# Performance work log

Hardware: AMD Instinct MI355X
Metric: run time of the kernel (lower is better)

Reference implementation:

```python
import jax, jax.numpy as jnp
import numpy as np
import math

HEADS = 16
SPH = 64      # size_per_head
KEY = 64      # key_size (defaults to size_per_head)
EMB = 1024
STEP = 3


def extract_seq_patches(x, kernel_size, step):
    # x: [B, L, D] -> [B, L, kernel_size, D]; patch j at pos t is x_pad[t - p_left + j*step]
    B, L, D = x.shape
    k_size = kernel_size + (step - 1) * (kernel_size - 1)
    p_right = (k_size - 1) // 2
    p_left = k_size - 1 - p_right
    xp = jnp.pad(x, ((0, 0), (p_left, p_right), (0, 0)))
    xs = [xp[:, i:i + L] for i in range(0, k_size, step)]  # kernel_size slices
    return jnp.stack(xs, axis=2)


def setup_inputs() -> dict:
    key = jax.random.key(0)
    kx, kq, kk, kv = jax.random.split(key, 4)
    B, L = 2, 4096
    x = jax.random.normal(kx, (B, L, EMB), dtype=jnp.float32)
    W_q = jax.random.normal(kq, (EMB, HEADS * KEY), dtype=jnp.float32) * 0.02
    W_k = jax.random.normal(kk, (EMB, HEADS * KEY), dtype=jnp.float32) * 0.02
    W_v = jax.random.normal(kv, (EMB, HEADS * SPH), dtype=jnp.float32) * 0.02
    return {"x": x, "W_q": W_q, "W_k": W_k, "W_v": W_v}


def _forward(x, W_q, W_k, W_v):
    B, L, D = x.shape
    pad_len = STEP - L % STEP
    x = jnp.pad(x, ((0, 0), (0, pad_len), (0, 0)))
    new_len = L + pad_len
    blocks = new_len // STEP
    q = x @ W_q  # [B, new_len, H*KEY]
    k = x @ W_k
    v = x @ W_v
    ksz = 1 + 2 * (STEP - 1)  # kernel_size = 5
    kp = extract_seq_patches(k, ksz, STEP)  # [B, new_len, ksz, H*KEY]
    vp = extract_seq_patches(v, ksz, STEP)
    # reshape to [B, H, step, blocks, d]
    q = q.reshape(B, blocks, STEP, HEADS, KEY).transpose(0, 3, 2, 1, 4)
    kb = k.reshape(B, blocks, STEP, HEADS, KEY).transpose(0, 3, 2, 1, 4)
    vb = v.reshape(B, blocks, STEP, HEADS, SPH).transpose(0, 3, 2, 1, 4)
    # neighbor patches: [B, H, step, blocks, ksz, d]
    kp = kp.reshape(B, blocks, STEP, ksz, HEADS, KEY).transpose(0, 4, 2, 1, 3, 5)
    vp = vp.reshape(B, blocks, STEP, ksz, HEADS, SPH).transpose(0, 4, 2, 1, 3, 5)
    scale = 1.0 / math.sqrt(KEY)
    # strided attention over blocks (same residue mod step): [B,H,step,blocks,blocks]
    a = jnp.einsum('bhsqk,bhspk->bhsqp', q, kb) * scale
    # block-local neighbor attention: [B,H,step,blocks,ksz]
    ap = jnp.einsum('bhsqk,bhsqnk->bhsqn', q, kp) * scale
    A = jax.nn.softmax(jnp.concatenate([a, ap], axis=-1), axis=-1)
    a, ap = A[..., :blocks], A[..., blocks:]
    o = (jnp.einsum('bhsqp,bhspd->bhsqd', a, vb)
         + jnp.einsum('bhsqn,bhsqnd->bhsqd', ap, vp))
    o = o.transpose(0, 3, 2, 1, 4).reshape(B, new_len, HEADS * SPH)
    return o[:, :L]


def reference(x, W_q, W_k, W_v):
    return _forward(x, W_q, W_k, W_v)
```

## Files before the change

kernel.cpp:

```cpp
#include <hip/hip_runtime.h>
#include <hip/hip_bf16.h>

typedef unsigned int u32;
typedef unsigned short u16;
typedef short s8v __attribute__((ext_vector_type(8)));
typedef short s4v __attribute__((ext_vector_type(4)));
typedef float f4v __attribute__((ext_vector_type(4)));
typedef float f16v __attribute__((ext_vector_type(16)));
typedef u32 u32x2 __attribute__((ext_vector_type(2)));
typedef u32 u32x4 __attribute__((ext_vector_type(4)));

#define NBLK 1366
#define VROW 1376
#define QSCALE 0.18033688011112042f

__device__ __forceinline__ u16 f2b(float f) {
  u32 u = __builtin_bit_cast(u32, f);
  u = (u + 0x7FFFu + ((u >> 16) & 1u)) >> 16;
  return (u16)u;
}

__device__ __forceinline__ u32 cvtpk(float a, float b) {
  u32 r;
  asm("v_cvt_pk_bf16_f32 %0, %1, %2" : "=v"(r) : "v"(a), "v"(b));
  return r;
}

__device__ __forceinline__ float fexp2(float x) {
#if defined(__has_builtin)
#if __has_builtin(__builtin_amdgcn_exp2f)
  return __builtin_amdgcn_exp2f(x);
#define FEXP2_DONE 1
#endif
#endif
#ifndef FEXP2_DONE
  float r;
  asm("v_exp_f32 %0, %1" : "=v"(r) : "v"(x));
  return r;
#endif
}

__device__ __forceinline__ f4v mfma32(s8v a, s8v b, f4v c) {
  return __builtin_amdgcn_mfma_f32_16x16x32_bf16(a, b, c, 0, 0, 0);
}

__device__ __forceinline__ f16v mfma3216(s8v a, s8v b, f16v c) {
  return __builtin_amdgcn_mfma_f32_32x32x16_bf16(a, b, c, 0, 0, 0);
}

__device__ __forceinline__ s4v lo4(s8v v) {
  return __builtin_shufflevector(v, v, 0, 1, 2, 3);
}
__device__ __forceinline__ s4v hi4(s8v v) {
  return __builtin_shufflevector(v, v, 4, 5, 6, 7);
}

__global__ __launch_bounds__(256) void k_prep(const float* __restrict__ x,
                                              const float* __restrict__ Wq,
                                              const float* __restrict__ Wk,
                                              const float* __restrict__ Wv,
                                              u16* __restrict__ xb,
                                              u16* __restrict__ Wt,
                                              u16* __restrict__ Vt) {
  const int bid = blockIdx.x;
  const int tid = threadIdx.x;
  if (bid < 4160) {
    long base = ((long)bid * 256 + tid) * 8;
    if (base >= 8320L * 1024L) return;
    int m = (int)(base >> 10);
    int c = (int)(base & 1023);
    int b = m / 4098;
    int t = m - b * 4098;
    s8v pack;
    if (m < 8196 && t < 4096) {
      const float* src = x + ((size_t)b * 4096 + t) * 1024 + c;
      float4 v0 = *(const float4*)(src);
      float4 v1 = *(const float4*)(src + 4);
      pack[0] = (short)f2b(v0.x); pack[1] = (short)f2b(v0.y);
      pack[2] = (short)f2b(v0.z); pack[3] = (short)f2b(v0.w);
      pack[4] = (short)f2b(v1.x); pack[5] = (short)f2b(v1.y);
      pack[6] = (short)f2b(v1.z); pack[7] = (short)f2b(v1.w);
    } else {
#pragma unroll
      for (int i = 0; i < 8; ++i) pack[i] = 0;
    }
    *(s8v*)(xb + base) = pack;
  } else if (bid < 7232) {
    __shared__ float tile[32][33];
    int bid3 = bid - 4160;
    int z = bid3 >> 10;
    int rem = bid3 & 1023;
    const float* W = (z == 0) ? Wq : ((z == 1) ? Wk : Wv);
    u16* dst = Wt + (size_t)z * 1024 * 1024;
    int n0 = (rem & 31) * 32, k0 = (rem >> 5) * 32;
    int tx = tid & 31, ty = tid >> 5;
#pragma unroll
    for (int i = 0; i < 4; ++i)
      tile[ty + i * 8][tx] = W[(size_t)(k0 + ty + i * 8) * 1024 + n0 + tx];
    __syncthreads();
#pragma unroll
    for (int i = 0; i < 4; ++i)
      dst[(size_t)(n0 + ty + i * 8) * 1024 + k0 + tx] = f2b(tile[tx][ty + i * 8]);
  } else {
    int gidx = (bid - 7232) * 256 + tid;
    if (gidx < 6144) {
      u16* dst = Vt + (size_t)gidx * VROW + NBLK;
#pragma unroll
      for (int i = 0; i < 10; ++i) dst[i] = 0;
    } else if (gidx < 6400) {
      Vt[(size_t)6144 * VROW + (gidx - 6144)] = 0;
    }
  }
}

__global__ __launch_bounds__(256, 4) void k_gemm_qkv(const u16* __restrict__ xb,
                                                     const u16* __restrict__ Wt,
                                                     u16* __restrict__ Qp,
                                                     u16* __restrict__ Kp,
                                                     u16* __restrict__ Vt) {
  const int wg = blockIdx.x;
  const int wid = (wg & 7) * 195 + (wg >> 3);
  const int mt = wid / 24;
  const int nz = wid - mt * 24;
  const int zid = nz >> 3;
  const int m0 = mt * 128;
  const int n0 = (nz & 7) * 128;
  const u16* Bg = Wt + (size_t)zid * 1024 * 1024 + (size_t)n0 * 1024;

  __shared__ __align__(16) u16 shl[16384];

  const int tid = threadIdx.x;
  const int lane = tid & 63;
  const int w = tid >> 6;
  const int wr = w >> 1, wc = w & 1;
  const int lo = lane & 15, g = lane >> 4;

  const int srow = tid >> 1;
  const int zsw = (tid >> 2) & 3;
  const int s0 = (tid & 1) * 2;
  const int c0 = s0 ^ zsw, c1 = (s0 + 1) ^ zsw;
  const int rsw = (g ^ ((lo >> 1) & 3)) << 4;

  f4v acc[4][4];
#pragma unroll
  for (int i = 0; i < 4; ++i)
#pragma unroll
    for (int j = 0; j < 4; ++j) {
      f4v z = {0.f, 0.f, 0.f, 0.f};
      acc[i][j] = z;
    }

  s8v ra0, ra1, rb0, rb1;
  auto load_regs = [&](int tile) {
    const int kt = tile * 32;
    const u16* ap = xb + (size_t)(m0 + srow) * 1024 + kt;
    ra0 = *(const s8v*)(ap + c0 * 8);
    ra1 = *(const s8v*)(ap + c1 * 8);
    const u16* bp = Bg + (size_t)srow * 1024 + kt;
    rb0 = *(const s8v*)(bp + c0 * 8);
    rb1 = *(const s8v*)(bp + c1 * 8);
  };

  auto stage_write = [&](int slot) {
    u16* Ab = shl + slot * 4096;
    u16* Bb = shl + 8192 + slot * 4096;
    *(s8v*)(Ab + srow * 32 + s0 * 8) = ra0;
    *(s8v*)(Ab + srow * 32 + s0 * 8 + 8) = ra1;
    *(s8v*)(Bb + srow * 32 + s0 * 8) = rb0;
    *(s8v*)(Bb + srow * 32 + s0 * 8 + 8) = rb1;
  };

  auto compute = [&](int slot) {
    const char* Ab = (const char*)(shl + slot * 4096);
    const char* Bb = (const char*)(shl + 8192 + slot * 4096);
    s8v af[4], bf[4];
#pragma unroll
    for (int i = 0; i < 4; ++i) {
      int ar = wr * 64 + i * 16 + lo;
      af[i] = *(const s8v*)(Ab + ar * 64 + rsw);
      int br = wc * 64 + i * 16 + lo;
      bf[i] = *(const s8v*)(Bb + br * 64 + rsw);
    }
    __builtin_amdgcn_s_setprio(1);
#pragma unroll
    for (int i = 0; i < 4; ++i)
#pragma unroll
      for (int j = 0; j < 4; ++j)
        acc[i][j] = mfma32(af[i], bf[j], acc[i][j]);
    __builtin_amdgcn_s_setprio(0);
  };

#define LGKM_BAR                                            \
  asm volatile("s_waitcnt lgkmcnt(0)" ::: "memory");        \
  __builtin_amdgcn_s_barrier();                             \
  asm volatile("" ::: "memory");

  load_regs(0);
  stage_write(0);
  load_regs(1);
  LGKM_BAR

#pragma unroll 1
  for (int t = 0; t < 31; ++t) {
    compute(t & 1);
    stage_write((t + 1) & 1);
    if (t < 30) load_regs(t + 2);
    LGKM_BAR
  }
  compute(1);
  __syncthreads();

#undef LGKM_BAR

  const float esc = (zid == 0) ? QSCALE : 1.0f;
  if (zid != 2) {
    u16* dq = (zid == 0) ? Qp : Kp;
#pragma unroll
    for (int i = 0; i < 4; ++i) {
#pragma unroll
      for (int r = 0; r < 4; ++r) {
        int m = m0 + wr * 64 + i * 16 + g * 4 + r;
        if (m >= 8196) continue;
        int b = m / 4098;
        int t = m - b * 4098;
        int s = t % 3;
        int p = t / 3;
        int cb = (b * 3 + s) * 16;
#pragma unroll
        for (int j = 0; j < 4; ++j) {
          int n = n0 + wc * 64 + j * 16 + lo;
          int h = n >> 6, d = n & 63;
          dq[(size_t)((cb + h) * NBLK + p) * 64 + d] = f2b(acc[i][j][r] * esc);
        }
      }
    }
  } else {
    u16* tile = shl;
#pragma unroll
    for (int i = 0; i < 4; ++i)
#pragma unroll
      for (int r = 0; r < 4; ++r) {
        int ml = wr * 64 + i * 16 + g * 4 + r;
#pragma unroll
        for (int j = 0; j < 4; ++j) {
          int nl = wc * 64 + j * 16 + lo;
          tile[ml * 128 + nl] = f2b(acc[i][j][r]);
        }
      }
    __syncthreads();
    for (int pair = tid; pair < 384; pair += 256) {
      int nl = pair & 127;
      int s = pair >> 7;
      int n = n0 + nl;
      int h = n >> 6, d = n & 63;
      for (int b = 0; b < 2; ++b) {
        int mlo = m0 > b * 4098 ? m0 : b * 4098;
        int cap = b * 4098 + 4096;
        int mhi = (m0 + 128 < cap) ? m0 + 128 : cap;
        if (mlo >= mhi) continue;
        int t_lo = mlo - b * 4098;
        int add = (s - (t_lo % 3) + 3) % 3;
        int t = t_lo + add;
        int tend = mhi - b * 4098;
        u16* dst = Vt + (size_t)(((b * 3 + s) * 16 + h) * 64 + d) * VROW;
        for (; t < tend; t += 3)
          dst[t / 3] = tile[(b * 4098 + t - m0) * 128 + nl];
      }
    }
  }
}

__global__ __launch_bounds__(256, 4) void k_attn(const u16* __restrict__ Qp,
                                                 const u16* __restrict__ Kp,
                                                 const u16* __restrict__ Vt,
                                                 float* __restrict__ out) {
  const int wg = blockIdx.x;
  const int idx = (wg & 7) * 132 + (wg >> 3);
  const int combo = idx / 11;
  const int qb = idx - combo * 11;
  const int b = combo / 48;
  const int rem = combo - b * 48;
  const int s = rem >> 4;
  const int h = rem & 15;
  const int tid = threadIdx.x, lane = tid & 63, w = tid >> 6;
  const int lq = lane & 31, lh = lane >> 5;

  const u16* Qg = Qp + (size_t)combo * (NBLK * 64);
  const u16* Kg = Kp + (size_t)combo * (NBLK * 64);
  const u16* Vg = Vt + (size_t)combo * (64 * VROW);

  __shared__ __align__(16) u16 att[2][4][64 * 36];

  const int qg = qb * 128 + w * 32 + lq;
  const int qc = (qg < NBLK) ? qg : (NBLK - 1);
  s8v qf[4];
#pragma unroll
  for (int ss = 0; ss < 4; ++ss)
    qf[ss] = *(const s8v*)(Qg + (size_t)qc * 64 + ss * 16 + lh * 8);

  f16v oacc0, oacc1;
#pragma unroll
  for (int i = 0; i < 16; ++i) { oacc0[i] = 0.f; oacc1[i] = 0.f; }
  float dpart[4] = {0.f, 0.f, 0.f, 0.f};

  const int srow = tid >> 2;
  const int sch = (tid & 3) * 2;
  const int ssub = (tid & 3) * 8;
  s8v kr0, kr1, vr0, vr1;

  auto load_regs = [&](int jt) {
    const int j0 = jt * 64;
    const u16* kp = Kg + (size_t)(j0 + srow) * 64 + sch * 8;
    kr0 = *(const s8v*)(kp);
    kr1 = *(const s8v*)(kp + 8);
    const u16* vp = Vg + (size_t)srow * VROW + j0 + sch * 8;
    vr0 = *(const s8v*)(vp);
    vr1 = *(const s8v*)(vp + 8);
  };

  auto stage_write = [&](int slot) {
    u16* K0 = att[slot][0];
    u16* K1 = att[slot][1];
    u16* V0 = att[slot][2];
    u16* V1 = att[slot][3];
    const int kb = srow * 36 + ssub;
    *(s4v*)(K0 + kb) = lo4(kr0);
    *(s4v*)(K0 + kb + 4) = hi4(kr0);
    *(s4v*)(K1 + kb) = lo4(kr1);
    *(s4v*)(K1 + kb + 4) = hi4(kr1);
    const int vb0 = srow * 36 + sch * 4;
    *(s4v*)(V0 + vb0) = lo4(vr0);
    *(s4v*)(V1 + vb0) = hi4(vr0);
    *(s4v*)(V0 + vb0 + 4) = lo4(vr1);
    *(s4v*)(V1 + vb0 + 4) = hi4(vr1);
  };

  const int qmin = qb * 128;

  auto compute = [&](int slot, int jt) {
    const int j0 = jt * 64;
    const u16* Kb = att[slot][lh];
    const u16* Vl0 = att[slot][2];
    const u16* Vl1 = att[slot][3];

    const bool special = ((j0 <= qmin + 130) && (j0 + 65 >= qmin)) || (j0 + 64 > NBLK);
#pragma unroll
    for (int jb = 0; jb < 2; ++jb) {
      f16v sacc;
#pragma unroll
      for (int i = 0; i < 16; ++i) sacc[i] = 0.f;
      __builtin_amdgcn_s_setprio(1);
#pragma unroll
      for (int ss = 0; ss < 4; ++ss) {
        const u16* kp = Kb + (jb * 32 + lq) * 36 + ss * 8;
        s4v a = *(const s4v*)kp;
        s4v b2 = *(const s4v*)(kp + 4);
        s8v kf = __builtin_shufflevector(a, b2, 0, 1, 2, 3, 4, 5, 6, 7);
        sacc = mfma3216(kf, qf[ss], sacc);
      }
      __builtin_amdgcn_s_setprio(0);

      float e[16];
      if (special) {
#pragma unroll
        for (int r = 0; r < 16; ++r) {
          int j = j0 + jb * 32 + (r & 3) + 8 * (r >> 2) + 4 * lh;
          float ev = fexp2(sacc[r]);
          int dd = j - qg;
          float fac = (j < NBLK) ? (((dd <= 2) && (dd >= -2)) ? 2.f : 1.f) : 0.f;
          e[r] = ev * fac;
        }
      } else {
#pragma unroll
        for (int r = 0; r < 16; ++r) e[r] = fexp2(sacc[r]);
      }
#pragma unroll
      for (int r = 0; r < 16; ++r) dpart[r & 3] += e[r];

#pragma unroll
      for (int g2 = 0; g2 < 2; ++g2) {
        u32 pe0 = cvtpk(e[g2 * 8 + 0], e[g2 * 8 + 1]);
        u32 pe1 = cvtpk(e[g2 * 8 + 2], e[g2 * 8 + 3]);
        u32 pe2 = cvtpk(e[g2 * 8 + 4], e[g2 * 8 + 5]);
        u32 pe3 = cvtpk(e[g2 * 8 + 6], e[g2 * 8 + 7]);
        asm("v_permlane32_swap_b32 %0, %1" : "+v"(pe0), "+v"(pe2));
        asm("v_permlane32_swap_b32 %0, %1" : "+v"(pe1), "+v"(pe3));
        u32x4 fw;
        fw[0] = pe0; fw[1] = pe1; fw[2] = pe2; fw[3] = pe3;
        s8v ef8 = __builtin_bit_cast(s8v, fw);
        const int ci = (jb * 4 + g2 * 2 + lh) * 4;
        s4v v0a = *(const s4v*)(Vl0 + lq * 36 + ci);
        s4v v0b = *(const s4v*)(Vl1 + lq * 36 + ci);
        s8v vf0 = __builtin_shufflevector(v0a, v0b, 0, 1, 2, 3, 4, 5, 6, 7);
        s4v v1a = *(const s4v*)(Vl0 + (32 + lq) * 36 + ci);
        s4v v1b = *(const s4v*)(Vl1 + (32 + lq) * 36 + ci);
        s8v vf1 = __builtin_shufflevector(v1a, v1b, 0, 1, 2, 3, 4, 5, 6, 7);
        __builtin_amdgcn_s_setprio(1);
        oacc0 = mfma3216(ef8, vf0, oacc0);
        oacc1 = mfma3216(ef8, vf1, oacc1);
        __builtin_amdgcn_s_setprio(0);
      }
    }
  };

#define LGKM_BAR                                            \
  asm volatile("s_waitcnt lgkmcnt(0)" ::: "memory");        \
  __builtin_amdgcn_s_barrier();                             \
  asm volatile("" ::: "memory");

  load_regs(0);
  stage_write(0);
  load_regs(1);
  LGKM_BAR

#pragma unroll 1
  for (int t = 0; t < 21; ++t) {
    compute(t & 1, t);
    stage_write((t + 1) & 1);
    if (t < 20) load_regs(t + 2);
    LGKM_BAR
  }
  compute(1, 21);

#undef LGKM_BAR

  float dtot = (dpart[0] + dpart[1]) + (dpart[2] + dpart[3]);
  dtot += __shfl_xor(dtot, 32, 64);

  const int hbase = h * 64;
#pragma unroll
  for (int r = 0; r < 16; ++r) {
    int cr = (r & 3) + 8 * (r >> 2) + 4 * lh;
    int q = qb * 128 + w * 32 + cr;
    float dq = __shfl(dtot, cr, 64);
    dq += (q == 0 || q == NBLK - 1) ? 2.f : ((q == 1 || q == NBLK - 2) ? 1.f : 0.f);
    float rr = 1.f / dq;
    int t = 3 * q + s;
    if (q < NBLK && t < 4096) {
      float* orow = out + ((size_t)b * 4096 + t) * 1024 + hbase + lq;
      orow[0] = oacc0[r] * rr;
      orow[32] = oacc1[r] * rr;
    }
  }
}

extern "C" void kernel_launch(void* const* d_in, const int* in_sizes, int n_in,
                              void* d_out, int out_size, void* d_ws, size_t ws_size,
                              hipStream_t stream) {
  const float* x  = (const float*)d_in[0];
  const float* Wq = (const float*)d_in[1];
  const float* Wk = (const float*)d_in[2];
  const float* Wv = (const float*)d_in[3];
  float* out = (float*)d_out;

  u16* ws = (u16*)d_ws;
  u16* xb = ws;
  u16* Wt = xb + 8519680;
  u16* Qp = Wt + 3145728;
  u16* Kp = Qp + 8392704;
  u16* Vt = Kp + 8392704;

  k_prep<<<dim3(7257), 256, 0, stream>>>(x, Wq, Wk, Wv, xb, Wt, Vt);
  k_gemm_qkv<<<dim3(1560), 256, 0, stream>>>(xb, Wt, Qp, Kp, Vt);
  k_attn<<<dim3(1056), 256, 0, stream>>>(Qp, Kp, Vt, out);
}
```

Before: 209.4 us.

## Load QKV GEMM MFMA fragments directly from global memory, dropping LDS staging

The QKV projection GEMM no longer stages A/B tiles through shared memory with barriers. Each wave now loads its MFMA fragments straight from global memory into double-buffered registers and alternates compute with prefetch of the next tile. Launch bounds are relaxed from 4 to 2 blocks per CU to make room for the larger register footprint. This removes LDS traffic and barrier synchronisation, but gives up cross-wave data sharing: each tile row is now fetched redundantly by two waves, relying on cache to absorb it, and occupancy may fall.

```diff
diff --git a/kernel.cpp b/kernel.cpp
--- a/kernel.cpp
+++ b/kernel.cpp
@@ -113,7 +113,7 @@
   }
 }
 
-__global__ __launch_bounds__(256, 4) void k_gemm_qkv(const u16* __restrict__ xb,
+__global__ __launch_bounds__(256, 2) void k_gemm_qkv(const u16* __restrict__ xb,
                                                      const u16* __restrict__ Wt,
                                                      u16* __restrict__ Qp,
                                                      u16* __restrict__ Kp,
@@ -135,12 +135,6 @@
   const int wr = w >> 1, wc = w & 1;
   const int lo = lane & 15, g = lane >> 4;
 
-  const int srow = tid >> 1;
-  const int zsw = (tid >> 2) & 3;
-  const int s0 = (tid & 1) * 2;
-  const int c0 = s0 ^ zsw, c1 = (s0 + 1) ^ zsw;
-  const int rsw = (g ^ ((lo >> 1) & 3)) << 4;
-
   f4v acc[4][4];
 #pragma unroll
   for (int i = 0; i < 4; ++i)
@@ -150,67 +144,62 @@
       acc[i][j] = z;
     }
 
-  s8v ra0, ra1, rb0, rb1;
-  auto load_regs = [&](int tile) {
-    const int kt = tile * 32;
-    const u16* ap = xb + (size_t)(m0 + srow) * 1024 + kt;
-    ra0 = *(const s8v*)(ap + c0 * 8);
-    ra1 = *(const s8v*)(ap + c1 * 8);
-    const u16* bp = Bg + (size_t)srow * 1024 + kt;
-    rb0 = *(const s8v*)(bp + c0 * 8);
-    rb1 = *(const s8v*)(bp + c1 * 8);
-  };
-
-  auto stage_write = [&](int slot) {
-    u16* Ab = shl + slot * 4096;
-    u16* Bb = shl + 8192 + slot * 4096;
-    *(s8v*)(Ab + srow * 32 + s0 * 8) = ra0;
-    *(s8v*)(Ab + srow * 32 + s0 * 8 + 8) = ra1;
-    *(s8v*)(Bb + srow * 32 + s0 * 8) = rb0;
-    *(s8v*)(Bb + srow * 32 + s0 * 8 + 8) = rb1;
-  };
-
-  auto compute = [&](int slot) {
-    const char* Ab = (const char*)(shl + slot * 4096);
-    const char* Bb = (const char*)(shl + 8192 + slot * 4096);
-    s8v af[4], bf[4];
+  const u16* ap[4];
+  const u16* bp[4];
+#pragma unroll
+  for (int i = 0; i < 4; ++i) {
+    ap[i] = xb + (size_t)(m0 + wr * 64 + i * 16 + lo) * 1024 + g * 8;
+    bp[i] = Bg + (size_t)(wc * 64 + i * 16 + lo) * 1024 + g * 8;
+  }
+
+  s8v a0[4], b0[4], a1[4], b1[4];
+
+  auto loadf0 = [&](int t) {
+    const int o = t * 32;
 #pragma unroll
     for (int i = 0; i < 4; ++i) {
-      int ar = wr * 64 + i * 16 + lo;
-      af[i] = *(const s8v*)(Ab + ar * 64 + rsw);
-      int br = wc * 64 + i * 16 + lo;
-      bf[i] = *(const s8v*)(Bb + br * 64 + rsw);
-    }
+      a0[i] = *(const s8v*)(ap[i] + o);
+      b0[i] = *(const s8v*)(bp[i] + o);
+    }
+  };
+  auto loadf1 = [&](int t) {
+    const int o = t * 32;
+#pragma unroll
+    for (int i = 0; i < 4; ++i) {
+      a1[i] = *(const s8v*)(ap[i] + o);
+      b1[i] = *(const s8v*)(bp[i] + o);
+    }
+  };
+  auto comp0 = [&]() {
     __builtin_amdgcn_s_setprio(1);
 #pragma unroll
     for (int i = 0; i < 4; ++i)
 #pragma unroll
       for (int j = 0; j < 4; ++j)
-        acc[i][j] = mfma32(af[i], bf[j], acc[i][j]);
+        acc[i][j] = mfma32(a0[i], b0[j], acc[i][j]);
     __builtin_amdgcn_s_setprio(0);
   };
-
-#define LGKM_BAR                                            \
-  asm volatile("s_waitcnt lgkmcnt(0)" ::: "memory");        \
-  __builtin_amdgcn_s_barrier();                             \
-  asm volatile("" ::: "memory");
-
-  load_regs(0);
-  stage_write(0);
-  load_regs(1);
-  LGKM_BAR
-
+  auto comp1 = [&]() {
+    __builtin_amdgcn_s_setprio(1);
+#pragma unroll
+    for (int i = 0; i < 4; ++i)
+#pragma unroll
+      for (int j = 0; j < 4; ++j)
+        acc[i][j] = mfma32(a1[i], b1[j], acc[i][j]);
+    __builtin_amdgcn_s_setprio(0);
+  };
+
+  loadf0(0);
+  loadf1(1);
 #pragma unroll 1
-  for (int t = 0; t < 31; ++t) {
-    compute(t & 1);
-    stage_write((t + 1) & 1);
-    if (t < 30) load_regs(t + 2);
-    LGKM_BAR
-  }
-  compute(1);
-  __syncthreads();
-
-#undef LGKM_BAR
+  for (int t = 0; t < 30; t += 2) {
+    comp0();
+    loadf0(t + 2);
+    comp1();
+    loadf1(t + 3);
+  }
+  comp0();
+  comp1();
 
   const float esc = (zid == 0) ? QSCALE : 1.0f;
   if (zid != 2) {
```

Measured after the change: 324.4 us. 1.55x slower.
